# Optimization experiments

Hardware: AMD Instinct MI355X
Metric: run time of the kernel (lower is better)

## Reference

```python
import jax, jax.numpy as jnp
import numpy as np

DEGREE = 3          # hardcoded in BSplineLoss
NUM_SAMPLES = 20    # hardcoded in BSplineLoss
B, N = 65536, 64


def setup_inputs() -> dict:
    key = jax.random.key(0)
    k1, k2 = jax.random.split(key)

    def make_seq(kk):
        ka, kb = jax.random.split(kk)
        # strictly increasing positive knots (valid B-spline knot vector)
        incr = jax.random.uniform(ka, (B, N), minval=0.1, maxval=1.0)
        knots = jnp.cumsum(incr, axis=1)
        coeffs = jax.random.normal(kb, (B, N, 2))
        return jnp.concatenate([knots[..., None], coeffs], axis=-1)  # [B,N,3]

    pred_seq = make_seq(k1)
    true_seq = make_seq(k2)
    true_masks = jnp.ones((B, N), dtype=jnp.int32)  # full-length splines
    return {"pred_seq": pred_seq, "true_seq": true_seq, "true_masks": true_masks}


def _deboor_sample(coeffs, knots):
    """Vectorized De Boor evaluation.
    coeffs: [B,n,2], knots: [B,n] -> samples [B,NUM_SAMPLES,2].
    Mirrors BSpline._interpolate with weights==1."""
    b, n, d = coeffs.shape
    dt = coeffs.dtype
    # prepend degree+1 zeros: full knot vector [B, n+degree+1]
    kf = jnp.concatenate([jnp.zeros((b, DEGREE + 1), dt), knots], axis=1)
    low = kf[:, DEGREE]          # knots[domain[0]]
    high = kf[:, n]              # knots[domain[1]] (domain[1] = n+degree - degree = n)
    t = jnp.linspace(0.0, 1.0, NUM_SAMPLES, dtype=dt)[None] * (high - low)[:, None] + low[:, None]  # [B,T]
    inner = kf[:, DEGREE:n]      # knots[domain[0]:domain[1]]
    s = jax.vmap(lambda a, v: jnp.searchsorted(a, v, side='right'))(inner, t) + DEGREE - 1  # [B,T]

    # homogeneous control points (weights = 1)
    v = jnp.concatenate([coeffs, jnp.ones((b, n, 1), dt)], axis=-1)  # [B,n,3]

    karr = jnp.arange(DEGREE + 1)               # local window index 0..degree
    idx = s[..., None] - DEGREE + karr          # [B,T,degree+1] global control indices
    bidx = jnp.arange(b)[:, None, None]
    p = v[bidx, idx]                            # [B,T,degree+1,3] local De Boor window

    for l in range(1, DEGREE + 1):  # l = degree+1 level does no work in the original
        ki = kf[bidx, idx]                       # knots[i]
        kj = kf[bidx, idx + DEGREE + 1 - l]      # knots[i+degree+1-l]
        denom = kj - ki
        safe = jnp.where(denom != 0, denom, jnp.ones((), dt))
        alpha = jnp.where(denom != 0, (t[..., None] - ki) / safe, jnp.zeros((), dt))  # [B,T,4]
        shifted = jnp.concatenate([p[:, :, :1], p[:, :, :-1]], axis=2)  # p[k-1]
        cand = (1.0 - alpha)[..., None] * shifted + alpha[..., None] * p
        p = jnp.where((karr >= l)[None, None, :, None], cand, p)

    return p[:, :, DEGREE, :d] / p[:, :, DEGREE, d:]  # [B,T,2]


def reference(pred_seq, true_seq, true_masks):
    pred_knots, pred_coeffs = pred_seq[:, :, 0], pred_seq[:, :, 1:3]
    true_knots, true_coeffs = true_seq[:, :, 0], true_seq[:, :, 1:3]
    # masks are all ones -> ragged selection is identity
    sampled_true = _deboor_sample(true_coeffs, true_knots)
    sampled_pred = _deboor_sample(pred_coeffs, pred_knots)
    mask = jnp.ones(sampled_true.shape[:2], sampled_true.dtype)  # [B,20]
    mse = (sampled_pred - sampled_true) ** 2
    return (mse * mask[..., None]).sum() / mask.sum()
```

## Files before the change

kernel.cpp:

```cpp
#include <hip/hip_runtime.h>

#define DEG 3
#define NSAMP 20
#define BROWS 65536
#define NKNOT 64
#define ROWS_PER_BLOCK 4
#define NBLOCKS (BROWS / ROWS_PER_BLOCK)

__global__ __launch_bounds__(256) void bspline_loss_main(
    const float* __restrict__ pred, const float* __restrict__ tru,
    float* __restrict__ partials)
{
    __shared__ float lds[ROWS_PER_BLOCK][2][192];
    __shared__ float wsum[ROWS_PER_BLOCK];

    const int tid  = threadIdx.x;
    const int wave = tid >> 6;
    const int lane = tid & 63;
    const int row  = blockIdx.x * ROWS_PER_BLOCK + wave;

    if (lane < 48) {
        const float4 p4 = ((const float4*)(pred + (size_t)row * 192))[lane];
        const float4 t4 = ((const float4*)(tru  + (size_t)row * 192))[lane];
        ((float4*)lds[wave][0])[lane] = p4;
        ((float4*)lds[wave][1])[lane] = t4;
    }
    __syncthreads();

    float rx = 0.f, ry = 0.f;
    if (lane < 40) {
        const int sel = (lane >= 20) ? 1 : 0;
        const int s   = sel ? lane - 20 : lane;
        const float* d = lds[wave][sel];

        const float high = d[3 * 60];
        const float t = ((float)s * (1.0f / 19.0f)) * high;

        int lo = 0, hi = 60;
        while (lo < hi) {
            int mid = (lo + hi) >> 1;
            if (d[3 * mid] <= t) lo = mid + 1; else hi = mid;
        }
        const int cnt = lo;

        float px[4], py[4], pw[4];
        #pragma unroll
        for (int k = 0; k < 4; ++k) {
            px[k] = d[3 * (cnt + k) + 1];
            py[k] = d[3 * (cnt + k) + 2];
            pw[k] = 1.0f;
        }
        #pragma unroll
        for (int l = 1; l <= DEG; ++l) {
            #pragma unroll
            for (int k = DEG; k >= l; --k) {
                const int i0 = cnt + k;
                const int i1 = cnt + k + (DEG + 1 - l);
                const float ki = (i0 < 4) ? 0.f : d[3 * (i0 - 4)];
                const float kj = (i1 < 4) ? 0.f : d[3 * (i1 - 4)];
                const float denom = kj - ki;
                const float alpha = (denom != 0.f) ? (t - ki) / denom : 0.f;
                const float b0 = 1.0f - alpha;
                px[k] = b0 * px[k - 1] + alpha * px[k];
                py[k] = b0 * py[k - 1] + alpha * py[k];
                pw[k] = b0 * pw[k - 1] + alpha * pw[k];
            }
        }
        rx = px[DEG] / pw[DEG];
        ry = py[DEG] / pw[DEG];
    }

    const float ox = __shfl(rx, lane + 20, 64);
    const float oy = __shfl(ry, lane + 20, 64);
    float acc = 0.f;
    if (lane < 20) {
        const float dx = rx - ox, dy = ry - oy;
        acc = dx * dx + dy * dy;
    }
    #pragma unroll
    for (int off = 32; off >= 1; off >>= 1)
        acc += __shfl_down(acc, off, 64);
    if (lane == 0) wsum[wave] = acc;
    __syncthreads();
    if (tid == 0)
        partials[blockIdx.x] = wsum[0] + wsum[1] + wsum[2] + wsum[3];
}

__global__ __launch_bounds__(256) void bspline_loss_reduce(
    const float* __restrict__ partials, float* __restrict__ out)
{
    const int tid = threadIdx.x;
    double acc = 0.0;
    const float4* p4 = (const float4*)partials;
    #pragma unroll 4
    for (int i = tid; i < NBLOCKS / 4; i += 256) {
        const float4 v = p4[i];
        acc += (double)v.x + (double)v.y + (double)v.z + (double)v.w;
    }
    #pragma unroll
    for (int off = 32; off >= 1; off >>= 1)
        acc += __shfl_down(acc, off, 64);
    __shared__ double ws[4];
    if ((tid & 63) == 0) ws[tid >> 6] = acc;
    __syncthreads();
    if (tid == 0) {
        const double tot = ws[0] + ws[1] + ws[2] + ws[3];
        out[0] = (float)(tot / (double)((long long)BROWS * NSAMP));
    }
}

extern "C" void kernel_launch(void* const* d_in, const int* in_sizes, int n_in,
                              void* d_out, int out_size, void* d_ws, size_t ws_size,
                              hipStream_t stream) {
    const float* pred = (const float*)d_in[0];
    const float* tru  = (const float*)d_in[1];
    float* out      = (float*)d_out;
    float* partials = (float*)d_ws;

    bspline_loss_main<<<NBLOCKS, 256, 0, stream>>>(pred, tru, partials);
    bspline_loss_reduce<<<1, 256, 0, stream>>>(partials, out);
}
```

Measured before the change: 133.3 us.

## Pack 8 rows per 320-thread block with full-lane sampling and branchless De Boor

Reorganizes the main kernel so each 320-thread block handles 8 rows, mapping every lane to a (row, sample, pred/true) slot instead of leaving 24 of 64 lanes idle per wave. The LDS layout is split into separate knot and float2 coefficient arrays. The binary search becomes an unrolled branchless search, and the De Boor recursion drops the homogeneous weight and uses a hardware reciprocal instead of a guarded divide. The pred/true pairing now uses a lane^32 shuffle, with the sum halved to correct for the double count. Risks: the non-vectorized strided global loads, the reciprocal's lower precision, and no zero-denominator guard.

```diff
diff --git a/kernel.cpp b/kernel.cpp
--- a/kernel.cpp
+++ b/kernel.cpp
@@ -1,89 +1,91 @@
 #include <hip/hip_runtime.h>
 
-#define DEG 3
-#define NSAMP 20
-#define BROWS 65536
-#define NKNOT 64
-#define ROWS_PER_BLOCK 4
-#define NBLOCKS (BROWS / ROWS_PER_BLOCK)
+#define NSAMP   20
+#define BROWS   65536
+#define RPB     8
+#define BLOCK   320
+#define NBLOCKS (BROWS / RPB)
 
-__global__ __launch_bounds__(256) void bspline_loss_main(
+__global__ __launch_bounds__(BLOCK) void bspline_loss_main(
     const float* __restrict__ pred, const float* __restrict__ tru,
     float* __restrict__ partials)
 {
-    __shared__ float lds[ROWS_PER_BLOCK][2][192];
-    __shared__ float wsum[ROWS_PER_BLOCK];
+    __shared__ float  kn[RPB][2][65];
+    __shared__ float2 cf[RPB][2][64];
+    __shared__ float  wpart[BLOCK / 64];
 
-    const int tid  = threadIdx.x;
-    const int wave = tid >> 6;
-    const int lane = tid & 63;
-    const int row  = blockIdx.x * ROWS_PER_BLOCK + wave;
+    const int tid = threadIdx.x;
+    const size_t base = (size_t)blockIdx.x * (RPB * 192);
 
-    if (lane < 48) {
-        const float4 p4 = ((const float4*)(pred + (size_t)row * 192))[lane];
-        const float4 t4 = ((const float4*)(tru  + (size_t)row * 192))[lane];
-        ((float4*)lds[wave][0])[lane] = p4;
-        ((float4*)lds[wave][1])[lane] = t4;
+    #pragma unroll
+    for (int tz = 0; tz < 2; ++tz) {
+        const float* src = (tz ? tru : pred) + base;
+        for (int j = tid; j < RPB * 64; j += BLOCK) {
+            const int row = j >> 6, q = j & 63;
+            const float k = src[3 * j];
+            const float x = src[3 * j + 1];
+            const float y = src[3 * j + 2];
+            kn[row][tz][q] = k;
+            cf[row][tz][q] = make_float2(x, y);
+        }
     }
     __syncthreads();
 
-    float rx = 0.f, ry = 0.f;
-    if (lane < 40) {
-        const int sel = (lane >= 20) ? 1 : 0;
-        const int s   = sel ? lane - 20 : lane;
-        const float* d = lds[wave][sel];
+    const int lane = tid & 63;
+    const int wave = tid >> 6;
+    const int slot = wave * 32 + (lane & 31);
+    const int sel  = lane >> 5;
+    const int row  = slot / 20;
+    const int s    = slot - row * 20;
 
-        const float high = d[3 * 60];
-        const float t = ((float)s * (1.0f / 19.0f)) * high;
+    const float*  K = kn[row][sel];
+    const float2* C = cf[row][sel];
 
-        int lo = 0, hi = 60;
-        while (lo < hi) {
-            int mid = (lo + hi) >> 1;
-            if (d[3 * mid] <= t) lo = mid + 1; else hi = mid;
-        }
-        const int cnt = lo;
+    const float high = K[60];
+    const float tv = (float)s * (1.0f / 19.0f) * high;
 
-        float px[4], py[4], pw[4];
-        #pragma unroll
-        for (int k = 0; k < 4; ++k) {
-            px[k] = d[3 * (cnt + k) + 1];
-            py[k] = d[3 * (cnt + k) + 2];
-            pw[k] = 1.0f;
-        }
-        #pragma unroll
-        for (int l = 1; l <= DEG; ++l) {
-            #pragma unroll
-            for (int k = DEG; k >= l; --k) {
-                const int i0 = cnt + k;
-                const int i1 = cnt + k + (DEG + 1 - l);
-                const float ki = (i0 < 4) ? 0.f : d[3 * (i0 - 4)];
-                const float kj = (i1 < 4) ? 0.f : d[3 * (i1 - 4)];
-                const float denom = kj - ki;
-                const float alpha = (denom != 0.f) ? (t - ki) / denom : 0.f;
-                const float b0 = 1.0f - alpha;
-                px[k] = b0 * px[k - 1] + alpha * px[k];
-                py[k] = b0 * py[k - 1] + alpha * py[k];
-                pw[k] = b0 * pw[k - 1] + alpha * pw[k];
-            }
-        }
-        rx = px[DEG] / pw[DEG];
-        ry = py[DEG] / pw[DEG];
+    int pos = 0;
+    #pragma unroll
+    for (int st = 32; st >= 1; st >>= 1)
+        pos += (K[pos + st - 1] <= tv) ? st : 0;
+    const int cnt = min(pos, 60);
+
+    float kfv[7];
+    #pragma unroll
+    for (int j = 1; j <= 6; ++j) {
+        const int idx = cnt + j - 4;
+        const float v = K[idx < 0 ? 0 : idx];
+        kfv[j] = (idx < 0) ? 0.f : v;
     }
 
-    const float ox = __shfl(rx, lane + 20, 64);
-    const float oy = __shfl(ry, lane + 20, 64);
-    float acc = 0.f;
-    if (lane < 20) {
-        const float dx = rx - ox, dy = ry - oy;
-        acc = dx * dx + dy * dy;
-    }
+    float2 p0 = C[cnt], p1 = C[cnt + 1], p2 = C[cnt + 2], p3 = C[cnt + 3];
+
+    auto alphaf = [&](float ki, float kj) {
+        return (tv - ki) * __builtin_amdgcn_rcpf(kj - ki);
+    };
+    auto lerp2 = [](float2 a, float2 b, float al) {
+        const float bl = 1.0f - al;
+        return make_float2(fmaf(al, b.x, bl * a.x), fmaf(al, b.y, bl * a.y));
+    };
+    p3 = lerp2(p2, p3, alphaf(kfv[3], kfv[6]));
+    p2 = lerp2(p1, p2, alphaf(kfv[2], kfv[5]));
+    p1 = lerp2(p0, p1, alphaf(kfv[1], kfv[4]));
+    p3 = lerp2(p2, p3, alphaf(kfv[3], kfv[5]));
+    p2 = lerp2(p1, p2, alphaf(kfv[2], kfv[4]));
+    p3 = lerp2(p2, p3, alphaf(kfv[3], kfv[4]));
+
+    const float ox = __shfl(p3.x, lane ^ 32, 64);
+    const float oy = __shfl(p3.y, lane ^ 32, 64);
+    const float dx = p3.x - ox, dy = p3.y - oy;
+    float acc = fmaf(dx, dx, dy * dy);
     #pragma unroll
     for (int off = 32; off >= 1; off >>= 1)
         acc += __shfl_down(acc, off, 64);
-    if (lane == 0) wsum[wave] = acc;
+    if (lane == 0) wpart[wave] = acc;
     __syncthreads();
     if (tid == 0)
-        partials[blockIdx.x] = wsum[0] + wsum[1] + wsum[2] + wsum[3];
+        partials[blockIdx.x] =
+            (wpart[0] + wpart[1] + wpart[2] + wpart[3] + wpart[4]) * 0.5f;
 }
 
 __global__ __launch_bounds__(256) void bspline_loss_reduce(
@@ -92,10 +94,10 @@
     const int tid = threadIdx.x;
     double acc = 0.0;
     const float4* p4 = (const float4*)partials;
-    #pragma unroll 4
+    #pragma unroll
     for (int i = tid; i < NBLOCKS / 4; i += 256) {
         const float4 v = p4[i];
-        acc += (double)v.x + (double)v.y + (double)v.z + (double)v.w;
+        acc += (double)((v.x + v.y) + (v.z + v.w));
     }
     #pragma unroll
     for (int off = 32; off >= 1; off >>= 1)
@@ -117,6 +119,6 @@
     float* out      = (float*)d_out;
     float* partials = (float*)d_ws;
 
-    bspline_loss_main<<<NBLOCKS, 256, 0, stream>>>(pred, tru, partials);
+    bspline_loss_main<<<NBLOCKS, BLOCK, 0, stream>>>(pred, tru, partials);
     bspline_loss_reduce<<<1, 256, 0, stream>>>(partials, out);
 }
```

Result: no change. 135.7 us (+1.8%).
